# Kernel tuning notes

Measured on AMD Instinct MI355X. Metric: run time of the kernel, lower is better.

Reference implementation:

```python
import jax, jax.numpy as jnp
import numpy as np

IN_MODES = (4, 4, 6, 8)  # prod = 768 = d_model; same modes for input and output
D_MODEL = 768
N_HEADS = 12
D_HEAD = D_MODEL // N_HEADS
SCALE = 1.0 / np.sqrt(D_HEAD)
TT_RANKS = (1, 32, 64, 32, 1)


def tt_linear(x, c0, c1, c2, c3, b):
    # TT-factorized linear: cores c_k have shape (r_{k-1}, m_k, n_k, r_k)
    # with in/out modes IN_MODES. x: [B, S, 768]
    B, S, D = x.shape
    t = x.reshape(B * S, *IN_MODES)                     # n i j k l over in-modes
    t = jnp.einsum('nijkl,mir->njklmr', t, c0[0])       # contract n1, r0=1 squeezed
    t = jnp.einsum('njklmr,rpjs->nklmps', t, c1)        # contract n2 and rank r1
    t = jnp.einsum('nklmps,sqkt->nlmpqt', t, c2)        # contract n3 and rank r2
    t = jnp.einsum('nlmpqt,tul->nmpqu', t, c3[..., 0])  # contract n4 and rank r3, r4=1
    return t.reshape(B, S, D) + b                        # out-modes m,p,q,u -> 768


def _make_tt_params(key):
    ks = jax.random.split(key, 4)
    cores = []
    for i in range(4):
        shape = (TT_RANKS[i], IN_MODES[i], IN_MODES[i], TT_RANKS[i + 1])
        cores.append(jax.random.normal(ks[i], shape, jnp.float32) * 0.05)
    bias = jnp.zeros((D_MODEL,), jnp.float32)
    return cores, bias


def setup_inputs() -> dict:
    key = jax.random.key(0)
    kx, kq, kk, kv, ko = jax.random.split(key, 5)
    B, S = 2, 2048
    x = jax.random.normal(kx, (B, S, D_MODEL), jnp.float32)
    mask = jnp.tril(jnp.ones((S, S), dtype=bool))[None, None]  # causal [1,1,S,S]
    out = {'x': x, 'mask': mask}
    for name, k in (('q', kq), ('k', kk), ('v', kv), ('o', ko)):
        cores, bias = _make_tt_params(k)
        for i in range(4):
            out[f'{name}c{i}'] = cores[i]
        out[f'{name}b'] = bias
    return out


def reference(x, mask,
              qc0, qc1, qc2, qc3, qb,
              kc0, kc1, kc2, kc3, kb,
              vc0, vc1, vc2, vc3, vb,
              oc0, oc1, oc2, oc3, ob):
    B, S, _ = x.shape
    q = tt_linear(x, qc0, qc1, qc2, qc3, qb)
    k = tt_linear(x, kc0, kc1, kc2, kc3, kb)
    v = tt_linear(x, vc0, vc1, vc2, vc3, vb)
    # [B, S, H, Dh] -> [B, H, S, Dh]
    q = q.reshape(B, S, N_HEADS, D_HEAD).transpose(0, 2, 1, 3)
    k = k.reshape(B, S, N_HEADS, D_HEAD).transpose(0, 2, 1, 3)
    v = v.reshape(B, S, N_HEADS, D_HEAD).transpose(0, 2, 1, 3)
    scores = jnp.einsum('bhqd,bhkd->bhqk', q, k) * SCALE  # full O(S^2) scores
    scores = jnp.where(mask, scores, jnp.float32(-10000.0))  # masked_fill(mask==0,-1e4)
    attn = jax.nn.softmax(scores, axis=-1)  # dropout is identity at eval
    out = jnp.einsum('bhqk,bhkd->bhqd', attn, v)
    out = out.transpose(0, 2, 1, 3).reshape(B, S, D_MODEL)
    return tt_linear(out, oc0, oc1, oc2, oc3, ob)
```

## Files before the change

### kernel.cpp

```cpp
#include <hip/hip_runtime.h>
#include <cstddef>
#include <cstdint>

#define D_MODEL 768
#define N_HEADS 12
#define SEQ 2048
#define BATCH 2
#define NROWS (BATCH * SEQ)
#define W_ELEMS (D_MODEL * D_MODEL)
#define Y_ELEMS (NROWS * D_MODEL)

typedef __attribute__((ext_vector_type(8))) short bf16x8;
typedef __attribute__((ext_vector_type(4))) float f32x4;

struct TTPtrs {
    const float* c0[4];
    const float* c1[4];
    const float* c2[4];
    const float* c3[4];
};

__device__ __forceinline__ float bf2f(uint16_t u) {
    union { uint32_t u; float f; } c; c.u = ((uint32_t)u) << 16; return c.f;
}
__device__ __forceinline__ uint16_t f2bf(float f) {
    union { float f; uint32_t u; } c; c.f = f;
    uint32_t x = c.u + 0x7fffu + ((c.u >> 16) & 1u);
    return (uint16_t)(x >> 16);
}
__device__ __forceinline__ uint32_t cvtpk(float lo, float hi) {
    uint32_t r;
    asm("v_cvt_pk_bf16_f32 %0, %1, %2" : "=v"(r) : "v"(lo), "v"(hi));
    return r;
}
__device__ __forceinline__ void glds16(const void* g, void* l) {
    auto gp = reinterpret_cast<const __attribute__((address_space(1))) uint32_t*>(
        reinterpret_cast<uintptr_t>(g));
    auto lp = reinterpret_cast<__attribute__((address_space(3))) uint32_t*>(
        reinterpret_cast<uintptr_t>(l));
    __builtin_amdgcn_global_load_lds(gp, lp, 16, 0, 0);
}

__global__ __launch_bounds__(256) void pre_kernel(TTPtrs P, float* __restrict__ wsA,
                                                  const float* __restrict__ x,
                                                  uint16_t* __restrict__ xb) {
    const int bx = blockIdx.x;
    if (bx < 256) {
        const int mat = bx >> 6;
        const float* c0 = P.c0[mat];
        const float* c1 = P.c1[mat];
        float* A = wsA + mat * 16384;
        int idx = (bx & 63) * 256 + threadIdx.x;
        int s = idx & 63, pj = (idx >> 6) & 15, mi = idx >> 10;
        float acc = 0.f;
        #pragma unroll 8
        for (int r = 0; r < 32; r++)
            acc = fmaf(c0[mi * 32 + r], c1[(r * 16 + pj) * 64 + s], acc);
        A[idx] = acc;
    } else {
        int idx = ((bx - 256) * 256 + threadIdx.x) * 4;
        float4 v = *(const float4*)(x + idx);
        *(uint2*)(xb + idx) = make_uint2(cvtpk(v.x, v.y), cvtpk(v.z, v.w));
    }
}

__global__ __launch_bounds__(256) void tt_buildB(TTPtrs P, const float* __restrict__ wsA,
                                                 float* __restrict__ wsB) {
    const int mat = blockIdx.y;
    const float* c2 = P.c2[mat];
    const float* A = wsA + mat * 16384;
    float* B = wsB + (size_t)mat * 294912;
    int idx = blockIdx.x * 256 + threadIdx.x;
    int t = idx & 31;
    int rest = idx >> 5;
    int qk = rest % 36;
    int rest2 = rest / 36;
    int pj = rest2 & 15, mi = rest2 >> 4;
    const float* Arow = A + (mi * 16 + pj) * 64;
    float acc = 0.f;
    #pragma unroll 8
    for (int s = 0; s < 64; s++)
        acc = fmaf(Arow[s], c2[(s * 36 + qk) * 32 + t], acc);
    B[idx] = acc;
}

__global__ __launch_bounds__(256) void tt_buildC(TTPtrs P, const float* __restrict__ wsB,
                                                 uint16_t* __restrict__ Wbf) {
    __shared__ float b_lds[36 * 33];
    __shared__ float c_lds[32 * 64];
    const int mat = blockIdx.y;
    const int mipj = blockIdx.x;
    const int mi = mipj >> 4, pj = mipj & 15;
    const int m = mi >> 2, i = mi & 3, p = pj >> 2, j = pj & 3;
    const float* Bsrc = wsB + (size_t)mat * 294912 + (size_t)mipj * 1152;
    const float* c3 = P.c3[mat];
    uint16_t* Wt = Wbf + (size_t)mat * W_ELEMS;
    const int tid = threadIdx.x;

    for (int e = tid; e < 1152; e += 256) {
        int qk = e >> 5, t = e & 31;
        b_lds[qk * 33 + t] = Bsrc[e];
    }
    for (int e = tid; e < 2048; e += 256)
        c_lds[e] = c3[e];
    __syncthreads();

    const int outbase = (m * 4 + p) * 48;
    const int inbase = (i * 4 + j) * 48;
    #pragma unroll
    for (int n = 0; n < 9; n++) {
        int idx = n * 256 + tid;
        int qu = idx / 48, kl = idx % 48;
        int q = qu >> 3, u = qu & 7, k = kl >> 3, l = kl & 7;
        const float* brow = &b_lds[(q * 6 + k) * 33];
        const float* crow = &c_lds[u * 8 + l];
        float acc = 0.f;
        #pragma unroll 8
        for (int t = 0; t < 32; t++)
            acc = fmaf(brow[t], crow[t * 64], acc);
        Wt[(size_t)(outbase + qu) * D_MODEL + inbase + kl] = f2bf(acc);
    }
}

template <int MODE>
__global__ __launch_bounds__(256) void gemm_mfma(const uint16_t* __restrict__ X,
                                                 const uint16_t* __restrict__ Wall,
                                                 const float* __restrict__ b0,
                                                 const float* __restrict__ b1,
                                                 const float* __restrict__ b2,
                                                 void* __restrict__ Yall,
                                                 uint16_t* __restrict__ Vt) {
    __shared__ uint16_t lds[2][8192];
    const int z = blockIdx.z;
    const uint16_t* W = Wall + (size_t)z * W_ELEMS;
    const float* bias = (z == 0) ? b0 : (z == 1 ? b1 : b2);
    const int m0 = blockIdx.x * 128, n0 = blockIdx.y * 128;
    const int tid = threadIdx.x, w = tid >> 6, l = tid & 63;
    const int wr = w >> 1, wc = w & 1;
    const int l15 = l & 15, lg = l >> 4;

    const int srow = w * 32 + (l >> 2);
    const int scol = ((l & 3) ^ ((l >> 2) & 3)) * 8;
    const uint16_t* Abase = X + (size_t)(m0 + srow) * D_MODEL + scol;
    const uint16_t* Bbase = W + (size_t)(n0 + srow) * D_MODEL + scol;

    f32x4 acc[4][4];
    #pragma unroll
    for (int mi = 0; mi < 4; ++mi)
        #pragma unroll
        for (int ni = 0; ni < 4; ++ni) acc[mi][ni] = (f32x4){0.f, 0.f, 0.f, 0.f};

    auto stage = [&](int buf, int kt) {
        const uint16_t* A0 = Abase + kt * 32;
        const uint16_t* B0 = Bbase + kt * 32;
        glds16(A0, &lds[buf][w * 1024]);
        glds16(A0 + 16 * D_MODEL, &lds[buf][w * 1024 + 512]);
        glds16(B0, &lds[buf][4096 + w * 1024]);
        glds16(B0 + 16 * D_MODEL, &lds[buf][4096 + w * 1024 + 512]);
    };

    stage(0, 0);
    __syncthreads();
    const int roff = ((lg ^ (l & 3)) << 3);
    for (int kt = 0; kt < 24; ++kt) {
        int cur = kt & 1;
        if (kt < 23) stage(cur ^ 1, kt + 1);
        const uint16_t* As = &lds[cur][0];
        const uint16_t* Bs = &lds[cur][4096];
        bf16x8 a[4], bb[4];
        #pragma unroll
        for (int mi = 0; mi < 4; ++mi)
            a[mi] = *(const bf16x8*)(As + (wr * 64 + mi * 16 + l15) * 32 + roff);
        #pragma unroll
        for (int ni = 0; ni < 4; ++ni)
            bb[ni] = *(const bf16x8*)(Bs + (wc * 64 + ni * 16 + l15) * 32 + roff);
        #pragma unroll
        for (int mi = 0; mi < 4; ++mi)
            #pragma unroll
            for (int ni = 0; ni < 4; ++ni)
                acc[mi][ni] = __builtin_amdgcn_mfma_f32_16x16x32_bf16(
                    a[mi], bb[ni], acc[mi][ni], 0, 0, 0);
        __syncthreads();
    }

    float bv[4];
    #pragma unroll
    for (int ni = 0; ni < 4; ++ni) bv[ni] = bias[n0 + wc * 64 + ni * 16 + l15];

    if (MODE == 1 && z == 2) {
        #pragma unroll
        for (int mi = 0; mi < 4; ++mi) {
            int row = m0 + wr * 64 + mi * 16 + lg * 4;
            int bb_ = row >> 11, s = row & 2047;
            #pragma unroll
            for (int ni = 0; ni < 4; ++ni) {
                int col = n0 + wc * 64 + ni * 16 + l15;
                float v0 = acc[mi][ni][0] + bv[ni], v1 = acc[mi][ni][1] + bv[ni];
                float v2 = acc[mi][ni][2] + bv[ni], v3 = acc[mi][ni][3] + bv[ni];
                *(uint2*)(Vt + ((size_t)(bb_ * 12 + (col >> 6)) * 64 + (col & 63)) * 2048 + s) =
                    make_uint2(cvtpk(v0, v1), cvtpk(v2, v3));
            }
        }
    } else {
        #pragma unroll
        for (int mi = 0; mi < 4; ++mi)
            #pragma unroll
            for (int ni = 0; ni < 4; ++ni)
                #pragma unroll
                for (int r = 0; r < 4; ++r) {
                    int row = m0 + wr * 64 + mi * 16 + lg * 4 + r;
                    int col = n0 + wc * 64 + ni * 16 + l15;
                    float v = acc[mi][ni][r] + bv[ni];
                    if (MODE == 1)
                        ((uint16_t*)Yall + (size_t)z * Y_ELEMS)[(size_t)row * D_MODEL + col] = f2bf(v);
                    else
                        ((float*)Yall)[(size_t)row * D_MODEL + col] = v;
                }
    }
}

__global__ __launch_bounds__(256) void attn_mfma(const uint16_t* __restrict__ Q,
                                                 const uint16_t* __restrict__ K,
                                                 const uint16_t* __restrict__ Vt,
                                                 uint16_t* __restrict__ O) {
    __shared__ uint16_t ks[2][4096];
    __shared__ uint16_t vs[2][4096];
    __shared__ uint16_t ps[4][1024];

    const int bx = blockIdx.x;
    const int qt = 31 - bx / 24;
    const int bh = bx % 24;
    const int b = bh / 12, h = bh % 12;
    const int tid = threadIdx.x, w = tid >> 6, l = tid & 63;
    const int l15 = l & 15, lg = l >> 4;
    const size_t headoff = (size_t)b * SEQ * D_MODEL + h * 64;
    const size_t vhead = ((size_t)(b * 12 + h)) << 17;
    const int sc8 = ((l & 7) ^ ((l >> 3) & 7)) * 8;
    const int srow = w * 16 + (l >> 3);

    const float QS = 0.125f * 1.44269504088896f;
    bf16x8 qf[2];
    {
        const uint16_t* qp = Q + headoff + (size_t)(qt * 64 + w * 16 + l15) * D_MODEL + lg * 8;
        #pragma unroll
        for (int ds = 0; ds < 2; ++ds) {
            bf16x8 qv = *(const bf16x8*)(qp + ds * 32);
            #pragma unroll
            for (int j = 0; j < 8; ++j)
                qf[ds][j] = (short)f2bf(bf2f((uint16_t)qv[j]) * QS);
        }
    }

    float m_ = -3e38f, l_ = 0.f;
    f32x4 oacc[4];
    #pragma unroll
    for (int ni = 0; ni < 4; ++ni) oacc[ni] = (f32x4){0.f, 0.f, 0.f, 0.f};
    const int qglob = qt * 64 + w * 16 + l15;

    auto stage = [&](int buf, int kt) {
        const uint16_t* ksrc = K + headoff + (size_t)(kt * 64 + srow) * D_MODEL + sc8;
        glds16(ksrc, &ks[buf][w * 1024]);
        glds16(ksrc + 8 * D_MODEL, &ks[buf][w * 1024 + 512]);
        const uint16_t* vsrc = Vt + vhead + (size_t)srow * SEQ + kt * 64 + sc8;
        glds16(vsrc, &vs[buf][w * 1024]);
        glds16(vsrc + 8 * SEQ, &vs[buf][w * 1024 + 512]);
    };

    stage(0, 0);
    for (int kt = 0; kt <= qt; ++kt) {
        const int cur = kt & 1;
        __syncthreads();
        if (kt < qt) stage(cur ^ 1, kt + 1);

        f32x4 sacc[4];
        #pragma unroll
        for (int ki = 0; ki < 4; ++ki) sacc[ki] = (f32x4){0.f, 0.f, 0.f, 0.f};
        __builtin_amdgcn_s_setprio(1);
        #pragma unroll
        for (int ds = 0; ds < 2; ++ds)
            #pragma unroll
            for (int ki = 0; ki < 4; ++ki) {
                int byte = (ki * 16 + l15) * 128 + ((((ds << 2) + lg) ^ (l15 & 7)) << 4);
                bf16x8 ak = *(const bf16x8*)((const char*)&ks[cur][0] + byte);
                sacc[ki] = __builtin_amdgcn_mfma_f32_16x16x32_bf16(ak, qf[ds], sacc[ki], 0, 0, 0);
            }
        __builtin_amdgcn_s_setprio(0);

        const bool diag = (kt == qt);
        float sv[16];
        float mx = -3e38f;
        #pragma unroll
        for (int ki = 0; ki < 4; ++ki)
            #pragma unroll
            for (int r = 0; r < 4; ++r) {
                float s = sacc[ki][r];
                if (diag) {
                    int key = kt * 64 + ki * 16 + lg * 4 + r;
                    if (key > qglob) s = -3e38f;
                }
                sv[ki * 4 + r] = s;
                mx = fmaxf(mx, s);
            }
        mx = fmaxf(mx, __shfl_xor(mx, 16));
        mx = fmaxf(mx, __shfl_xor(mx, 32));
        if (__any(mx > m_ + 11.54f)) {
            float mnew = fmaxf(m_, mx);
            float alpha = __builtin_amdgcn_exp2f(m_ - mnew);
            l_ *= alpha;
            float a0 = __shfl(alpha, lg * 4 + 0), a1 = __shfl(alpha, lg * 4 + 1);
            float a2 = __shfl(alpha, lg * 4 + 2), a3 = __shfl(alpha, lg * 4 + 3);
            #pragma unroll
            for (int ni = 0; ni < 4; ++ni) {
                oacc[ni][0] *= a0; oacc[ni][1] *= a1;
                oacc[ni][2] *= a2; oacc[ni][3] *= a3;
            }
            m_ = mnew;
        }
        float sum = 0.f;
        uint32_t pk[8];
        #pragma unroll
        for (int i = 0; i < 16; i += 2) {
            float p0 = __builtin_amdgcn_exp2f(sv[i] - m_);
            float p1 = __builtin_amdgcn_exp2f(sv[i + 1] - m_);
            sum += p0 + p1;
            pk[i >> 1] = cvtpk(p0, p1);
        }
        sum += __shfl_xor(sum, 16);
        sum += __shfl_xor(sum, 32);
        l_ += sum;

        uint16_t* psw = &ps[w][0];
        #pragma unroll
        for (int ki = 0; ki < 4; ++ki) {
            int byte = (l15 * 128 + ki * 32 + lg * 8) ^ ((l15 & 7) << 4);
            *(uint2*)((char*)psw + byte) = make_uint2(pk[ki * 2], pk[ki * 2 + 1]);
        }
        asm volatile("s_waitcnt lgkmcnt(0)" ::: "memory");
        __builtin_amdgcn_sched_barrier(0);

        __builtin_amdgcn_s_setprio(1);
        #pragma unroll
        for (int kss = 0; kss < 2; ++kss) {
            int pbyte = l15 * 128 + ((((kss << 2) + lg) ^ (l15 & 7)) << 4);
            bf16x8 ap = *(const bf16x8*)((const char*)psw + pbyte);
            #pragma unroll
            for (int ni = 0; ni < 4; ++ni) {
                int vbyte = (ni * 16 + l15) * 128 + ((((kss << 2) + lg) ^ (l15 & 7)) << 4);
                bf16x8 bv = *(const bf16x8*)((const char*)&vs[cur][0] + vbyte);
                oacc[ni] = __builtin_amdgcn_mfma_f32_16x16x32_bf16(ap, bv, oacc[ni], 0, 0, 0);
            }
        }
        __builtin_amdgcn_s_setprio(0);
    }

    float li0 = 1.f / __shfl(l_, lg * 4 + 0), li1 = 1.f / __shfl(l_, lg * 4 + 1);
    float li2 = 1.f / __shfl(l_, lg * 4 + 2), li3 = 1.f / __shfl(l_, lg * 4 + 3);
    #pragma unroll
    for (int ni = 0; ni < 4; ++ni) {
        int col = h * 64 + ni * 16 + l15;
        size_t rb = (size_t)(b * SEQ + qt * 64 + w * 16 + lg * 4) * D_MODEL + col;
        O[rb + 0 * D_MODEL] = f2bf(oacc[ni][0] * li0);
        O[rb + 1 * D_MODEL] = f2bf(oacc[ni][1] * li1);
        O[rb + 2 * D_MODEL] = f2bf(oacc[ni][2] * li2);
        O[rb + 3 * D_MODEL] = f2bf(oacc[ni][3] * li3);
    }
}

extern "C" void kernel_launch(void* const* d_in, const int* in_sizes, int n_in,
                              void* d_out, int out_size, void* d_ws, size_t ws_size,
                              hipStream_t stream) {
    const float* x = (const float*)d_in[0];
    TTPtrs P;
    const float* biases[4];
    const int base[4] = {2, 7, 12, 17};
    for (int t = 0; t < 4; t++) {
        P.c0[t] = (const float*)d_in[base[t] + 0];
        P.c1[t] = (const float*)d_in[base[t] + 1];
        P.c2[t] = (const float*)d_in[base[t] + 2];
        P.c3[t] = (const float*)d_in[base[t] + 3];
        biases[t] = (const float*)d_in[base[t] + 4];
    }

    char* ws = (char*)d_ws;
    float* wsA = (float*)(ws + 0);
    float* wsB = (float*)(ws + 262144);
    uint16_t* Wbf = (uint16_t*)(ws + 4980736);
    uint16_t* xbf = (uint16_t*)(ws + 9699328);
    uint16_t* Qbf = (uint16_t*)(ws + 15990784);
    uint16_t* Kbf = (uint16_t*)(ws + 22282240);
    uint16_t* Vtbf = (uint16_t*)(ws + 28573696);
    uint16_t* Obf = (uint16_t*)(ws + 34865152);
    (void)Kbf;

    pre_kernel<<<dim3(256 + 3072), 256, 0, stream>>>(P, wsA, x, xbf);
    tt_buildB<<<dim3(1152, 4), 256, 0, stream>>>(P, wsA, wsB);
    tt_buildC<<<dim3(256, 4), 256, 0, stream>>>(P, wsB, Wbf);

    gemm_mfma<1><<<dim3(32, 6, 3), 256, 0, stream>>>(xbf, Wbf, biases[0], biases[1],
                                                     biases[2], (void*)Qbf, Vtbf);
    attn_mfma<<<dim3(24 * 32), 256, 0, stream>>>(Qbf, Kbf, Vtbf, Obf);

    gemm_mfma<0><<<dim3(32, 6, 1), 256, 0, stream>>>(Obf, Wbf + 3 * (size_t)W_ELEMS,
                                                     biases[3], biases[3], biases[3],
                                                     d_out, nullptr);
}
```

Baseline: 239.8 us.

## Split causal attention over key chunks and merge partials in a combine kernel

The causal attention kernel is split-K: each query tile's key range is cut into chunks of at most 8 key tiles, giving 1920 blocks of roughly equal work instead of 768 blocks whose loop lengths range from 1 to 32 tiles. Each block writes a normalized bf16 partial output and its log-sum-exp into scratch (reusing the output buffer and the x-bf16 workspace). A new combine kernel then merges the partials with softmax weights into the attention output. The aim is to fix load imbalance and the long tail from diagonal ordering, at the cost of an extra launch, extra global traffic, and a second bf16 rounding of the partials.

```diff
diff --git a/kernel.cpp b/kernel.cpp
--- a/kernel.cpp
+++ b/kernel.cpp
@@ -222,14 +222,26 @@
 __global__ __launch_bounds__(256) void attn_mfma(const uint16_t* __restrict__ Q,
                                                  const uint16_t* __restrict__ K,
                                                  const uint16_t* __restrict__ Vt,
-                                                 uint16_t* __restrict__ O) {
+                                                 uint16_t* __restrict__ pO1,
+                                                 uint16_t* __restrict__ pO2,
+                                                 float* __restrict__ tbuf) {
     __shared__ uint16_t ks[2][4096];
     __shared__ uint16_t vs[2][4096];
     __shared__ uint16_t ps[4][1024];
 
     const int bx = blockIdx.x;
-    const int qt = 31 - bx / 24;
+    const int u = bx / 24;
     const int bh = bx % 24;
+    int g, c;
+    if (u < 32)      { g = u >> 2,            c = u & 3; }
+    else if (u < 56) { int t = u - 32; g = 8 + t / 3,  c = t % 3; }
+    else if (u < 72) { int t = u - 56; g = 16 + (t >> 1), c = t & 1; }
+    else             { g = 24 + (u - 72),     c = 0; }
+    const int qt = 31 - g;
+    const int ktlo = c * 8;
+    const int kthi = min(ktlo + 7, qt);
+    const int nkt = kthi - ktlo + 1;
+
     const int b = bh / 12, h = bh % 12;
     const int tid = threadIdx.x, w = tid >> 6, l = tid & 63;
     const int l15 = l & 15, lg = l >> 4;
@@ -266,11 +278,12 @@
         glds16(vsrc + 8 * SEQ, &vs[buf][w * 1024 + 512]);
     };
 
-    stage(0, 0);
-    for (int kt = 0; kt <= qt; ++kt) {
-        const int cur = kt & 1;
+    stage(0, ktlo);
+    for (int it = 0; it < nkt; ++it) {
+        const int kt = ktlo + it;
+        const int cur = it & 1;
         __syncthreads();
-        if (kt < qt) stage(cur ^ 1, kt + 1);
+        if (it + 1 < nkt) stage(cur ^ 1, kt + 1);
 
         f32x4 sacc[4];
         #pragma unroll
@@ -288,7 +301,6 @@
 
         const bool diag = (kt == qt);
         float sv[16];
-        float mx = -3e38f;
         #pragma unroll
         for (int ki = 0; ki < 4; ++ki)
             #pragma unroll
@@ -299,8 +311,11 @@
                     if (key > qglob) s = -3e38f;
                 }
                 sv[ki * 4 + r] = s;
-                mx = fmaxf(mx, s);
             }
+        float mx = fmaxf(fmaxf(sv[0], sv[1]), sv[2]);
+        #pragma unroll
+        for (int i = 3; i < 15; i += 2) mx = fmaxf(fmaxf(mx, sv[i]), sv[i + 1]);
+        mx = fmaxf(mx, sv[15]);
         mx = fmaxf(mx, __shfl_xor(mx, 16));
         mx = fmaxf(mx, __shfl_xor(mx, 32));
         if (__any(mx > m_ + 11.54f)) {
@@ -355,15 +370,69 @@
 
     float li0 = 1.f / __shfl(l_, lg * 4 + 0), li1 = 1.f / __shfl(l_, lg * 4 + 1);
     float li2 = 1.f / __shfl(l_, lg * 4 + 2), li3 = 1.f / __shfl(l_, lg * 4 + 3);
+    uint16_t* op = (bx < 1536) ? (pO1 + (size_t)bx * 4096)
+                               : (pO2 + (size_t)(bx - 1536) * 4096);
     #pragma unroll
     for (int ni = 0; ni < 4; ++ni) {
-        int col = h * 64 + ni * 16 + l15;
-        size_t rb = (size_t)(b * SEQ + qt * 64 + w * 16 + lg * 4) * D_MODEL + col;
-        O[rb + 0 * D_MODEL] = f2bf(oacc[ni][0] * li0);
-        O[rb + 1 * D_MODEL] = f2bf(oacc[ni][1] * li1);
-        O[rb + 2 * D_MODEL] = f2bf(oacc[ni][2] * li2);
-        O[rb + 3 * D_MODEL] = f2bf(oacc[ni][3] * li3);
-    }
+        int col = ni * 16 + l15;
+        int rbase = (w * 16 + lg * 4) * 64 + col;
+        op[rbase + 0 * 64] = f2bf(oacc[ni][0] * li0);
+        op[rbase + 1 * 64] = f2bf(oacc[ni][1] * li1);
+        op[rbase + 2 * 64] = f2bf(oacc[ni][2] * li2);
+        op[rbase + 3 * 64] = f2bf(oacc[ni][3] * li3);
+    }
+    if (lg == 0)
+        tbuf[(size_t)bx * 64 + w * 16 + l15] = m_ + __log2f(l_);
+}
+
+__global__ __launch_bounds__(256) void attn_combine(const uint16_t* __restrict__ pO1,
+                                                    const uint16_t* __restrict__ pO2,
+                                                    const float* __restrict__ tbuf,
+                                                    uint16_t* __restrict__ Obf) {
+    __shared__ float t_lds[4][64];
+    const int bx = blockIdx.x;
+    const int qt = bx & 31, bh = bx >> 5;
+    const int b = bh / 12, h = bh % 12;
+    const int g = 31 - qt;
+    const int u_base = (g < 8) ? 4 * g : (g < 16) ? 32 + 3 * (g - 8)
+                     : (g < 24) ? 56 + 2 * (g - 16) : 72 + (g - 24);
+    const int nc = (g < 8) ? 4 : (g < 16) ? 3 : (g < 24) ? 2 : 1;
+    const int tid = threadIdx.x;
+    if (tid < nc * 64) {
+        int c = tid >> 6, q = tid & 63;
+        t_lds[c][q] = tbuf[(size_t)((u_base + c) * 24 + bh) * 64 + q];
+    }
+    __syncthreads();
+
+    const int q = tid >> 2, d0 = (tid & 3) * 16;
+    float tmax = t_lds[0][q];
+    for (int c = 1; c < nc; ++c) tmax = fmaxf(tmax, t_lds[c][q]);
+    float acc[16];
+    #pragma unroll
+    for (int j = 0; j < 16; ++j) acc[j] = 0.f;
+    float denom = 0.f;
+    for (int c = 0; c < nc; ++c) {
+        float wgt = __builtin_amdgcn_exp2f(t_lds[c][q] - tmax);
+        denom += wgt;
+        int ug = (u_base + c) * 24 + bh;
+        const uint16_t* op = (ug < 1536) ? (pO1 + (size_t)ug * 4096)
+                                         : (pO2 + (size_t)(ug - 1536) * 4096);
+        bf16x8 v0 = *(const bf16x8*)(op + q * 64 + d0);
+        bf16x8 v1 = *(const bf16x8*)(op + q * 64 + d0 + 8);
+        #pragma unroll
+        for (int j = 0; j < 8; ++j) {
+            acc[j]     += bf2f((uint16_t)v0[j]) * wgt;
+            acc[8 + j] += bf2f((uint16_t)v1[j]) * wgt;
+        }
+    }
+    float inv = 1.f / denom;
+    uint32_t outp[8];
+    #pragma unroll
+    for (int j = 0; j < 8; ++j)
+        outp[j] = cvtpk(acc[2 * j] * inv, acc[2 * j + 1] * inv);
+    size_t rb = (size_t)(b * SEQ + qt * 64 + q) * D_MODEL + h * 64 + d0;
+    *(uint4*)(Obf + rb)     = make_uint4(outp[0], outp[1], outp[2], outp[3]);
+    *(uint4*)(Obf + rb + 8) = make_uint4(outp[4], outp[5], outp[6], outp[7]);
 }
 
 extern "C" void kernel_launch(void* const* d_in, const int* in_sizes, int n_in,
@@ -386,10 +455,13 @@
     float* wsB = (float*)(ws + 262144);
     uint16_t* Wbf = (uint16_t*)(ws + 4980736);
     uint16_t* xbf = (uint16_t*)(ws + 9699328);
+    uint16_t* pO2 = (uint16_t*)(ws + 9699328);
+    float* tbuf = (float*)(ws + 12845056);
     uint16_t* Qbf = (uint16_t*)(ws + 15990784);
     uint16_t* Kbf = (uint16_t*)(ws + 22282240);
     uint16_t* Vtbf = (uint16_t*)(ws + 28573696);
     uint16_t* Obf = (uint16_t*)(ws + 34865152);
+    uint16_t* pO1 = (uint16_t*)d_out;
     (void)Kbf;
 
     pre_kernel<<<dim3(256 + 3072), 256, 0, stream>>>(P, wsA, x, xbf);
@@ -398,7 +470,8 @@
 
     gemm_mfma<1><<<dim3(32, 6, 3), 256, 0, stream>>>(xbf, Wbf, biases[0], biases[1],
                                                      biases[2], (void*)Qbf, Vtbf);
-    attn_mfma<<<dim3(24 * 32), 256, 0, stream>>>(Qbf, Kbf, Vtbf, Obf);
+    attn_mfma<<<dim3(1920), 256, 0, stream>>>(Qbf, Kbf, Vtbf, pO1, pO2, tbuf);
+    attn_combine<<<dim3(768), 256, 0, stream>>>(pO1, pO2, tbuf, Obf);
 
     gemm_mfma<0><<<dim3(32, 6, 1), 256, 0, stream>>>(Obf, Wbf + 3 * (size_t)W_ELEMS,
                                                      biases[3], biases[3], biases[3],
```

New measurement: 237.5 us. About the same (-1.0%).
